# Kernel optimization log

Measured on AMD Instinct MI355X. Metric: run time of the kernel, lower is better.

## Reference

```python
import jax, jax.numpy as jnp
import numpy as np

L, D, OC, GROUPS, EPS = 256, 1280, 128, 8, 1e-5


def setup_inputs() -> dict:
    key = jax.random.key(0)
    k1, k2 = jax.random.split(key)
    feats = jax.random.normal(k1, (L, D), dtype=jnp.float32)
    # Conv2d(3d, out_ch, kernel_size=1) weight flattened to (out_ch, 3d)
    W = jax.random.normal(k2, (OC, 3 * D), dtype=jnp.float32) * (1.0 / np.sqrt(3 * D))
    b = jnp.zeros((OC,), dtype=jnp.float32)
    gamma = jnp.ones((OC,), dtype=jnp.float32)
    beta = jnp.zeros((OC,), dtype=jnp.float32)
    return {"feats": feats, "W": W, "b": b, "gamma": gamma, "beta": beta}


def reference(feats, W, b, gamma, beta):
    fi = feats[:, None, :]                     # (L, 1, d)
    fj = feats[None, :, :]                     # (1, L, d)
    add = fi + fj                              # (L, L, d)
    diff = jnp.abs(fi - fj)                    # (L, L, d)
    had = fi * fj                              # (L, L, d)
    pair = jnp.concatenate([add, diff, had], axis=-1)  # (L, L, 3d)
    # 1x1 conv == per-pixel linear: (L, L, 3d) x (out_ch, 3d)^T -> (L, L, out_ch)
    x = jnp.einsum('ijc,oc->ijo', pair, W) + b
    # GroupNorm(8, out_ch) on batch=1: normalize over (C/g, L, L) per group
    xg = jnp.transpose(x, (2, 0, 1)).reshape(GROUPS, OC // GROUPS, L, L)
    mean = jnp.mean(xg, axis=(1, 2, 3), keepdims=True)
    var = jnp.var(xg, axis=(1, 2, 3), keepdims=True)
    xn = ((xg - mean) * jax.lax.rsqrt(var + EPS)).reshape(OC, L, L)
    xn = xn * gamma[:, None, None] + beta[:, None, None]
    out = jax.nn.gelu(xn, approximate=False)   # torch nn.GELU default = exact erf
    return out[None]                           # (1, out_ch, L, L)
```

## Files before the change

### kernel.cpp

```cpp
#include <hip/hip_runtime.h>
#include <math.h>

typedef unsigned int uint;
typedef unsigned short ushort;

typedef __attribute__((ext_vector_type(8))) _Float16 f16x8;
typedef __attribute__((ext_vector_type(2))) _Float16 f16x2;
typedef __attribute__((ext_vector_type(16))) float floatx16;

#define NFEAT 327680
#define NWA   163840
#define NWP   327680

union U4H8 { uint4 u; f16x8 h; uint w[4]; };

__device__ inline ushort f2h(float f) {
  _Float16 h = (_Float16)f;
  union { _Float16 h; ushort s; } c; c.h = h; return c.s;
}
__device__ inline f16x2 asf16x2(uint u) {
  union { uint u; f16x2 h; } c; c.u = u; return c.h;
}
__device__ inline uint asuint(f16x2 h) {
  union { f16x2 h; uint u; } c; c.h = h; return c.u;
}

__global__ void prep_kernel(const float* __restrict__ feats,
                            const float* __restrict__ W,
                            ushort* __restrict__ fH,
                            ushort* __restrict__ wA,
                            ushort* __restrict__ wP,
                            float* __restrict__ stats,
                            float* __restrict__ Aoi) {
  int idx = blockIdx.x * 256 + threadIdx.x;
  if (blockIdx.x == 0 && threadIdx.x < 16) stats[threadIdx.x] = 0.0f;
  if (idx < 32768) Aoi[idx] = 0.0f;
  if (idx < NFEAT) {
    fH[idx] = f2h(feats[idx]);
  } else {
    const int e = idx - NFEAT;
    const int o = e / 3840;
    const int c = e - o * 3840;
    const ushort v = f2h(W[e]);
    if (c < 1280) {
      wA[o * 1280 + c] = v;
    } else {
      const int cp = c - 1280;
      const int t = cp / 1280;
      const int kk = cp - t * 1280;
      const int ks = kk >> 4;
      const int khalf = (kk >> 3) & 1;
      const int ko = kk & 7;
      const int lane = khalf * 32 + (o & 31);
      const int tile = (ks * 2 + t) * 4 + (o >> 5);
      wP[tile * 512 + lane * 8 + ko] = v;
    }
  }
}

__global__ __launch_bounds__(256, 2) void gemma_kernel(
    const ushort* __restrict__ fH, const ushort* __restrict__ wA,
    float* __restrict__ Aoi) {
  __shared__ float red[4][1024];
  const int tid = threadIdx.x, lane = tid & 63, w = tid >> 6;
  const int i0 = (blockIdx.x >> 4) << 5;
  const int kq = (blockIdx.x >> 2) & 3;
  const int ot = blockIdx.x & 3;
  const int rr = lane & 31, half = lane >> 5;
  floatx16 a4;
  #pragma unroll
  for (int r = 0; r < 16; ++r) a4[r] = 0.0f;
  const int kbase = kq * 320 + w * 80 + half * 8;
  #pragma unroll
  for (int ks = 0; ks < 5; ++ks) {
    const int k = kbase + ks * 16;
    U4H8 bf; bf.u = *(const uint4*)(fH + (i0 + rr) * 1280 + k);
    U4H8 af; af.u = *(const uint4*)(wA + (ot * 32 + rr) * 1280 + k);
    a4 = __builtin_amdgcn_mfma_f32_32x32x16_f16(af.h, bf.h, a4, 0, 0, 0);
  }
  #pragma unroll
  for (int r = 0; r < 16; ++r) {
    const int orow = (r & 3) + 8 * (r >> 2) + 4 * half;
    red[w][orow * 32 + rr] = a4[r];
  }
  __syncthreads();
  for (int e = tid; e < 1024; e += 256) {
    float s = red[0][e] + red[1][e] + red[2][e] + red[3][e];
    atomicAdd(&Aoi[(ot * 32 + (e >> 5)) * 256 + i0 + (e & 31)], s);
  }
}

__device__ inline void build_pair(const uint4 vj, const uint4 vi, U4H8& d, U4H8& h) {
  const uint ju[4] = {vj.x, vj.y, vj.z, vj.w};
  const uint iu[4] = {vi.x, vi.y, vi.z, vi.w};
  #pragma unroll
  for (int t = 0; t < 4; ++t) {
    f16x2 a = asf16x2(iu[t]);
    f16x2 b = asf16x2(ju[t]);
    f16x2 dd = a - b;
    f16x2 hh = a * b;
    d.w[t] = asuint(dd) & 0x7fff7fffu;
    h.w[t] = asuint(hh);
  }
}

__global__ __launch_bounds__(256, 2) void gemm_kernel(
    const ushort* __restrict__ fH, const ushort* __restrict__ wP,
    const float* __restrict__ bias, const float* __restrict__ Aoi,
    float* __restrict__ xout, float* __restrict__ stats) {
  __shared__ float sred[16];

  const int tid = threadIdx.x;
  const int blk = blockIdx.x;
  const int i0 = (blk >> 2) << 1;
  const int j0 = (blk & 3) << 6;
  const int lane = tid & 63;
  const int w = tid >> 6;
  const int wo = (w >> 1) << 6;
  const int wm = (w & 1) << 5;
  const int rr = lane & 31;
  const int half = lane >> 5;

  const ushort* wpl = wP + ((wo >> 5) << 9) + lane * 8;
  const ushort* fi0p = fH + i0 * 1280 + half * 8;
  const ushort* fi1p = fi0p + 1280;
  const ushort* fjp  = fH + (j0 + wm + rr) * 1280 + half * 8;

  floatx16 acc[2][2];
  #pragma unroll
  for (int a = 0; a < 2; ++a)
    #pragma unroll
    for (int ot = 0; ot < 2; ++ot)
      #pragma unroll
      for (int r = 0; r < 16; ++r) acc[a][ot][r] = 0.0f;

  U4H8 wfA[8], wfB[8];
  uint4 vjA[2], viA0[2], viA1[2], vjB[2], viB0[2], viB1[2];

#define CHUNK_LOAD(WF, VJ, VI0, VI1, CC) do {                                 \
    const int _b = (CC) * 16;                                                 \
    _Pragma("unroll")                                                         \
    for (int _q = 0; _q < 8; ++_q) {                                          \
      const int _st = _q >> 2, _t = (_q >> 1) & 1, _oi = _q & 1;              \
      (WF)[_q].u = *(const uint4*)(wpl + ((_b + _st * 8 + _t * 4 + _oi) << 9)); \
    }                                                                         \
    const int _cb = (CC) << 5;                                                \
    _Pragma("unroll")                                                         \
    for (int _s = 0; _s < 2; ++_s) {                                          \
      (VJ)[_s]  = *(const uint4*)(fjp  + _cb + _s * 16);                      \
      (VI0)[_s] = *(const uint4*)(fi0p + _cb + _s * 16);                      \
      (VI1)[_s] = *(const uint4*)(fi1p + _cb + _s * 16);                      \
    }                                                                         \
  } while (0)

#define CHUNK_COMPUTE(WF, VJ, VI0, VI1) do {                                  \
    _Pragma("unroll")                                                         \
    for (int _s = 0; _s < 2; ++_s) {                                          \
      U4H8 d0, h0, d1, h1;                                                    \
      build_pair((VJ)[_s], (VI0)[_s], d0, h0);                                \
      build_pair((VJ)[_s], (VI1)[_s], d1, h1);                                \
      acc[0][0] = __builtin_amdgcn_mfma_f32_32x32x16_f16((WF)[_s*4+0].h, d0.h, acc[0][0], 0, 0, 0); \
      acc[1][0] = __builtin_amdgcn_mfma_f32_32x32x16_f16((WF)[_s*4+0].h, d1.h, acc[1][0], 0, 0, 0); \
      acc[0][1] = __builtin_amdgcn_mfma_f32_32x32x16_f16((WF)[_s*4+1].h, d0.h, acc[0][1], 0, 0, 0); \
      acc[1][1] = __builtin_amdgcn_mfma_f32_32x32x16_f16((WF)[_s*4+1].h, d1.h, acc[1][1], 0, 0, 0); \
      acc[0][0] = __builtin_amdgcn_mfma_f32_32x32x16_f16((WF)[_s*4+2].h, h0.h, acc[0][0], 0, 0, 0); \
      acc[1][0] = __builtin_amdgcn_mfma_f32_32x32x16_f16((WF)[_s*4+2].h, h1.h, acc[1][0], 0, 0, 0); \
      acc[0][1] = __builtin_amdgcn_mfma_f32_32x32x16_f16((WF)[_s*4+3].h, h0.h, acc[0][1], 0, 0, 0); \
      acc[1][1] = __builtin_amdgcn_mfma_f32_32x32x16_f16((WF)[_s*4+3].h, h1.h, acc[1][1], 0, 0, 0); \
    }                                                                         \
  } while (0)

  CHUNK_LOAD(wfA, vjA, viA0, viA1, 0);
  #pragma unroll 1
  for (int cc = 0; cc < 40; cc += 2) {
    CHUNK_LOAD(wfB, vjB, viB0, viB1, cc + 1);
    CHUNK_COMPUTE(wfA, vjA, viA0, viA1);
    if (cc + 2 < 40)
      CHUNK_LOAD(wfA, vjA, viA0, viA1, cc + 2);
    CHUNK_COMPUTE(wfB, vjB, viB0, viB1);
  }
#undef CHUNK_LOAD
#undef CHUNK_COMPUTE

  float gs[2][2] = {{0.f, 0.f}, {0.f, 0.f}};
  float gq[2][2] = {{0.f, 0.f}, {0.f, 0.f}};
  const int jg = j0 + wm + rr;
  #pragma unroll
  for (int ii = 0; ii < 2; ++ii) {
    const int irow = i0 + ii;
    const int mglob = irow * 256 + jg;
    #pragma unroll
    for (int ot = 0; ot < 2; ++ot) {
      #pragma unroll
      for (int r = 0; r < 16; ++r) {
        const int orow = (r & 3) + 8 * (r >> 2) + 4 * half;
        const int o = wo + ot * 32 + orow;
        float x = acc[ii][ot][r] + Aoi[o * 256 + irow] + Aoi[o * 256 + jg] + bias[o];
        xout[o * 65536 + mglob] = x;
        gs[ot][r >> 3] += x;
        gq[ot][r >> 3] += x * x;
      }
    }
  }
  if (tid < 16) sred[tid] = 0.0f;
  __syncthreads();
  #pragma unroll
  for (int ot = 0; ot < 2; ++ot) {
    #pragma unroll
    for (int rg = 0; rg < 2; ++rg) {
      float s = gs[ot][rg], qv = gq[ot][rg];
      for (int off = 32; off > 0; off >>= 1) {
        s += __shfl_xor(s, off, 64);
        qv += __shfl_xor(qv, off, 64);
      }
      if (lane == 0) {
        const int g = (wo >> 4) + ot * 2 + rg;
        atomicAdd(&sred[g], s);
        atomicAdd(&sred[8 + g], qv);
      }
    }
  }
  __syncthreads();
  if (tid < 16) atomicAdd(&stats[tid], sred[tid]);
}

__global__ void norm_kernel(float* __restrict__ xout,
                            const float* __restrict__ stats,
                            const float* __restrict__ gamma,
                            const float* __restrict__ beta) {
  const int idx = blockIdx.x * 256 + threadIdx.x;
  const int e = idx << 2;
  const int o = e >> 16;
  const int g = o >> 4;
  const float invN = 1.0f / 1048576.0f;
  const float mean = stats[g] * invN;
  const float var = stats[8 + g] * invN - mean * mean;
  const float inv = rsqrtf(var + 1e-5f);
  const float ga = gamma[o], be = beta[o];
  float4 v = *(float4*)(xout + e);
  float* pv = &v.x;
  #pragma unroll
  for (int t = 0; t < 4; ++t) {
    float xn = (pv[t] - mean) * inv * ga + be;
    pv[t] = 0.5f * xn * (1.0f + erff(xn * 0.70710678118654752f));
  }
  *(float4*)(xout + e) = v;
}

extern "C" void kernel_launch(void* const* d_in, const int* in_sizes, int n_in,
                              void* d_out, int out_size, void* d_ws, size_t ws_size,
                              hipStream_t stream) {
  const float* feats = (const float*)d_in[0];
  const float* W     = (const float*)d_in[1];
  const float* bias  = (const float*)d_in[2];
  const float* gamma = (const float*)d_in[3];
  const float* beta  = (const float*)d_in[4];
  float* out = (float*)d_out;

  ushort* fH = (ushort*)d_ws;
  ushort* wA = fH + NFEAT;
  ushort* wP = wA + NWA;
  float* stats = (float*)(wP + NWP);
  float* Aoi = stats + 16;

  prep_kernel<<<3200, 256, 0, stream>>>(feats, W, fH, wA, wP, stats, Aoi);
  gemma_kernel<<<128, 256, 0, stream>>>(fH, wA, Aoi);
  gemm_kernel<<<512, 256, 0, stream>>>(fH, wP, bias, Aoi, out, stats);
  norm_kernel<<<8192, 256, 0, stream>>>(out, stats, gamma, beta);
}
```

Measured before the change: 144.4 us.

## Fuse GroupNorm+GELU into GEMM via cooperative grid sync, keeping tile in registers

Merges the normalization kernel into the GEMM kernel using a cooperative launch and grid-wide sync, so pre-norm values stay in accumulator registers instead of being written and reread from global memory. Blocks grow to 512 threads covering four i-rows each, halving the grid to 256 blocks so all can be co-resident. Saves a full-size output round trip and one launch, at the cost of a grid barrier, tighter launch bounds that may pressure registers, and live accumulators across the sync.

```diff
diff --git a/kernel.cpp b/kernel.cpp
--- a/kernel.cpp
+++ b/kernel.cpp
@@ -1,5 +1,8 @@
 #include <hip/hip_runtime.h>
+#include <hip/hip_cooperative_groups.h>
 #include <math.h>
+
+namespace cg = cooperative_groups;
 
 typedef unsigned int uint;
 typedef unsigned short ushort;
@@ -104,25 +107,29 @@
   }
 }
 
-__global__ __launch_bounds__(256, 2) void gemm_kernel(
+__global__ __launch_bounds__(512, 4) void gemm_kernel(
     const ushort* __restrict__ fH, const ushort* __restrict__ wP,
     const float* __restrict__ bias, const float* __restrict__ Aoi,
-    float* __restrict__ xout, float* __restrict__ stats) {
+    float* __restrict__ xout, float* __restrict__ stats,
+    const float* __restrict__ gamma, const float* __restrict__ beta) {
   __shared__ float sred[16];
 
   const int tid = threadIdx.x;
   const int blk = blockIdx.x;
-  const int i0 = (blk >> 2) << 1;
+  const int i0 = (blk >> 2) << 2;
   const int j0 = (blk & 3) << 6;
   const int lane = tid & 63;
   const int w = tid >> 6;
-  const int wo = (w >> 1) << 6;
-  const int wm = (w & 1) << 5;
+  const int p  = w >> 2;
+  const int ob = (w >> 1) & 1;
+  const int jb = w & 1;
+  const int wo = ob << 6;
+  const int wm = jb << 5;
   const int rr = lane & 31;
   const int half = lane >> 5;
 
   const ushort* wpl = wP + ((wo >> 5) << 9) + lane * 8;
-  const ushort* fi0p = fH + i0 * 1280 + half * 8;
+  const ushort* fi0p = fH + (i0 + p * 2) * 1280 + half * 8;
   const ushort* fi1p = fi0p + 1280;
   const ushort* fjp  = fH + (j0 + wm + rr) * 1280 + half * 8;
 
@@ -187,8 +194,7 @@
   const int jg = j0 + wm + rr;
   #pragma unroll
   for (int ii = 0; ii < 2; ++ii) {
-    const int irow = i0 + ii;
-    const int mglob = irow * 256 + jg;
+    const int irow = i0 + p * 2 + ii;
     #pragma unroll
     for (int ot = 0; ot < 2; ++ot) {
       #pragma unroll
@@ -196,7 +202,7 @@
         const int orow = (r & 3) + 8 * (r >> 2) + 4 * half;
         const int o = wo + ot * 32 + orow;
         float x = acc[ii][ot][r] + Aoi[o * 256 + irow] + Aoi[o * 256 + jg] + bias[o];
-        xout[o * 65536 + mglob] = x;
+        acc[ii][ot][r] = x;
         gs[ot][r >> 3] += x;
         gq[ot][r >> 3] += x * x;
       }
@@ -222,29 +228,37 @@
   }
   __syncthreads();
   if (tid < 16) atomicAdd(&stats[tid], sred[tid]);
-}
-
-__global__ void norm_kernel(float* __restrict__ xout,
-                            const float* __restrict__ stats,
-                            const float* __restrict__ gamma,
-                            const float* __restrict__ beta) {
-  const int idx = blockIdx.x * 256 + threadIdx.x;
-  const int e = idx << 2;
-  const int o = e >> 16;
-  const int g = o >> 4;
+
+  cg::this_grid().sync();
+
   const float invN = 1.0f / 1048576.0f;
-  const float mean = stats[g] * invN;
-  const float var = stats[8 + g] * invN - mean * mean;
-  const float inv = rsqrtf(var + 1e-5f);
-  const float ga = gamma[o], be = beta[o];
-  float4 v = *(float4*)(xout + e);
-  float* pv = &v.x;
-  #pragma unroll
-  for (int t = 0; t < 4; ++t) {
-    float xn = (pv[t] - mean) * inv * ga + be;
-    pv[t] = 0.5f * xn * (1.0f + erff(xn * 0.70710678118654752f));
-  }
-  *(float4*)(xout + e) = v;
+  float gmean[2][2], ginv[2][2];
+  #pragma unroll
+  for (int ot = 0; ot < 2; ++ot)
+    #pragma unroll
+    for (int rg = 0; rg < 2; ++rg) {
+      const int g = (wo >> 4) + ot * 2 + rg;
+      const float mean = stats[g] * invN;
+      const float var = stats[8 + g] * invN - mean * mean;
+      gmean[ot][rg] = mean;
+      ginv[ot][rg] = rsqrtf(var + 1e-5f);
+    }
+  #pragma unroll
+  for (int ii = 0; ii < 2; ++ii) {
+    const int irow = i0 + p * 2 + ii;
+    const int mglob = irow * 256 + jg;
+    #pragma unroll
+    for (int ot = 0; ot < 2; ++ot) {
+      #pragma unroll
+      for (int r = 0; r < 16; ++r) {
+        const int orow = (r & 3) + 8 * (r >> 2) + 4 * half;
+        const int o = wo + ot * 32 + orow;
+        float xn = (acc[ii][ot][r] - gmean[ot][r >> 3]) * ginv[ot][r >> 3] * gamma[o] + beta[o];
+        xout[o * 65536 + mglob] =
+            0.5f * xn * (1.0f + erff(xn * 0.70710678118654752f));
+      }
+    }
+  }
 }
 
 extern "C" void kernel_launch(void* const* d_in, const int* in_sizes, int n_in,
@@ -265,6 +279,8 @@
 
   prep_kernel<<<3200, 256, 0, stream>>>(feats, W, fH, wA, wP, stats, Aoi);
   gemma_kernel<<<128, 256, 0, stream>>>(fH, wA, Aoi);
-  gemm_kernel<<<512, 256, 0, stream>>>(fH, wP, bias, Aoi, out, stats);
-  norm_kernel<<<8192, 256, 0, stream>>>(out, stats, gamma, beta);
-}
+
+  void* args[] = {&fH, &wP, &bias, &Aoi, &out, &stats, &gamma, &beta};
+  hipLaunchCooperativeKernel((void*)gemm_kernel, dim3(256), dim3(512),
+                             args, 0, stream);
+}
```

Result: slower. 375.0 us (+159.7%).

## Enlarge per-wave GEMM tile to 2i x 64j x 64o for more register reuse

Applied to the files above, without the earlier changes.

Each wave now computes a 2x2 tile of i-rows by j-subblocks across two 32-output slices, doubling accumulators to 8 MFMA tiles. Each weight fragment and pair-feature build is reused across more MFMAs, cutting global weight/feature loads per FLOP. The block covers 4 i-rows, so the grid halves to 256 blocks, and launch bounds drop to 1 block/SM to allow more registers. The risk is lower occupancy and fewer blocks than CUs, which may hurt latency hiding and load balance.

```diff
diff --git a/kernel.cpp b/kernel.cpp
--- a/kernel.cpp
+++ b/kernel.cpp
@@ -104,7 +104,7 @@
   }
 }
 
-__global__ __launch_bounds__(256, 2) void gemm_kernel(
+__global__ __launch_bounds__(256, 1) void gemm_kernel(
     const ushort* __restrict__ fH, const ushort* __restrict__ wP,
     const float* __restrict__ bias, const float* __restrict__ Aoi,
     float* __restrict__ xout, float* __restrict__ stats) {
@@ -112,32 +112,37 @@
 
   const int tid = threadIdx.x;
   const int blk = blockIdx.x;
-  const int i0 = (blk >> 2) << 1;
-  const int j0 = (blk & 3) << 6;
   const int lane = tid & 63;
   const int w = tid >> 6;
-  const int wo = (w >> 1) << 6;
-  const int wm = (w & 1) << 5;
+  const int ip = w >> 1;
+  const int ot = w & 1;
+  const int i0 = (blk >> 2) * 4 + ip * 2;
+  const int j0 = (blk & 3) << 6;
+  const int wo = ot << 6;
   const int rr = lane & 31;
   const int half = lane >> 5;
 
   const ushort* wpl = wP + ((wo >> 5) << 9) + lane * 8;
   const ushort* fi0p = fH + i0 * 1280 + half * 8;
   const ushort* fi1p = fi0p + 1280;
-  const ushort* fjp  = fH + (j0 + wm + rr) * 1280 + half * 8;
-
-  floatx16 acc[2][2];
+  const ushort* fj0p = fH + (j0 + rr) * 1280 + half * 8;
+  const ushort* fj1p = fj0p + 32 * 1280;
+
+  floatx16 acc[2][2][2];
   #pragma unroll
   for (int a = 0; a < 2; ++a)
     #pragma unroll
-    for (int ot = 0; ot < 2; ++ot)
+    for (int b = 0; b < 2; ++b)
       #pragma unroll
-      for (int r = 0; r < 16; ++r) acc[a][ot][r] = 0.0f;
+      for (int c = 0; c < 2; ++c)
+        #pragma unroll
+        for (int r = 0; r < 16; ++r) acc[a][b][c][r] = 0.0f;
 
   U4H8 wfA[8], wfB[8];
-  uint4 vjA[2], viA0[2], viA1[2], vjB[2], viB0[2], viB1[2];
-
-#define CHUNK_LOAD(WF, VJ, VI0, VI1, CC) do {                                 \
+  uint4 vj0A[2], vj1A[2], vi0A[2], vi1A[2];
+  uint4 vj0B[2], vj1B[2], vi0B[2], vi1B[2];
+
+#define CHUNK_LOAD(WF, VJ0, VJ1, VI0, VI1, CC) do {                           \
     const int _b = (CC) * 16;                                                 \
     _Pragma("unroll")                                                         \
     for (int _q = 0; _q < 8; ++_q) {                                          \
@@ -147,74 +152,85 @@
     const int _cb = (CC) << 5;                                                \
     _Pragma("unroll")                                                         \
     for (int _s = 0; _s < 2; ++_s) {                                          \
-      (VJ)[_s]  = *(const uint4*)(fjp  + _cb + _s * 16);                      \
+      (VJ0)[_s] = *(const uint4*)(fj0p + _cb + _s * 16);                      \
+      (VJ1)[_s] = *(const uint4*)(fj1p + _cb + _s * 16);                      \
       (VI0)[_s] = *(const uint4*)(fi0p + _cb + _s * 16);                      \
       (VI1)[_s] = *(const uint4*)(fi1p + _cb + _s * 16);                      \
     }                                                                         \
   } while (0)
 
-#define CHUNK_COMPUTE(WF, VJ, VI0, VI1) do {                                  \
+#define CHUNK_COMPUTE(WF, VJ0, VJ1, VI0, VI1) do {                            \
     _Pragma("unroll")                                                         \
     for (int _s = 0; _s < 2; ++_s) {                                          \
-      U4H8 d0, h0, d1, h1;                                                    \
-      build_pair((VJ)[_s], (VI0)[_s], d0, h0);                                \
-      build_pair((VJ)[_s], (VI1)[_s], d1, h1);                                \
-      acc[0][0] = __builtin_amdgcn_mfma_f32_32x32x16_f16((WF)[_s*4+0].h, d0.h, acc[0][0], 0, 0, 0); \
-      acc[1][0] = __builtin_amdgcn_mfma_f32_32x32x16_f16((WF)[_s*4+0].h, d1.h, acc[1][0], 0, 0, 0); \
-      acc[0][1] = __builtin_amdgcn_mfma_f32_32x32x16_f16((WF)[_s*4+1].h, d0.h, acc[0][1], 0, 0, 0); \
-      acc[1][1] = __builtin_amdgcn_mfma_f32_32x32x16_f16((WF)[_s*4+1].h, d1.h, acc[1][1], 0, 0, 0); \
-      acc[0][0] = __builtin_amdgcn_mfma_f32_32x32x16_f16((WF)[_s*4+2].h, h0.h, acc[0][0], 0, 0, 0); \
-      acc[1][0] = __builtin_amdgcn_mfma_f32_32x32x16_f16((WF)[_s*4+2].h, h1.h, acc[1][0], 0, 0, 0); \
-      acc[0][1] = __builtin_amdgcn_mfma_f32_32x32x16_f16((WF)[_s*4+3].h, h0.h, acc[0][1], 0, 0, 0); \
-      acc[1][1] = __builtin_amdgcn_mfma_f32_32x32x16_f16((WF)[_s*4+3].h, h1.h, acc[1][1], 0, 0, 0); \
+      U4H8 d00, h00, d01, h01, d10, h10, d11, h11;                            \
+      build_pair((VJ0)[_s], (VI0)[_s], d00, h00);                             \
+      build_pair((VJ0)[_s], (VI1)[_s], d01, h01);                             \
+      build_pair((VJ1)[_s], (VI0)[_s], d10, h10);                             \
+      build_pair((VJ1)[_s], (VI1)[_s], d11, h11);                             \
+      _Pragma("unroll")                                                       \
+      for (int _oi = 0; _oi < 2; ++_oi) {                                     \
+        const f16x8 wd = (WF)[_s * 4 + _oi].h;                                \
+        const f16x8 wh = (WF)[_s * 4 + 2 + _oi].h;                            \
+        acc[0][0][_oi] = __builtin_amdgcn_mfma_f32_32x32x16_f16(wd, d00.h, acc[0][0][_oi], 0, 0, 0); \
+        acc[1][0][_oi] = __builtin_amdgcn_mfma_f32_32x32x16_f16(wd, d01.h, acc[1][0][_oi], 0, 0, 0); \
+        acc[0][1][_oi] = __builtin_amdgcn_mfma_f32_32x32x16_f16(wd, d10.h, acc[0][1][_oi], 0, 0, 0); \
+        acc[1][1][_oi] = __builtin_amdgcn_mfma_f32_32x32x16_f16(wd, d11.h, acc[1][1][_oi], 0, 0, 0); \
+        acc[0][0][_oi] = __builtin_amdgcn_mfma_f32_32x32x16_f16(wh, h00.h, acc[0][0][_oi], 0, 0, 0); \
+        acc[1][0][_oi] = __builtin_amdgcn_mfma_f32_32x32x16_f16(wh, h01.h, acc[1][0][_oi], 0, 0, 0); \
+        acc[0][1][_oi] = __builtin_amdgcn_mfma_f32_32x32x16_f16(wh, h10.h, acc[0][1][_oi], 0, 0, 0); \
+        acc[1][1][_oi] = __builtin_amdgcn_mfma_f32_32x32x16_f16(wh, h11.h, acc[1][1][_oi], 0, 0, 0); \
+      }                                                                       \
     }                                                                         \
   } while (0)
 
-  CHUNK_LOAD(wfA, vjA, viA0, viA1, 0);
+  CHUNK_LOAD(wfA, vj0A, vj1A, vi0A, vi1A, 0);
   #pragma unroll 1
   for (int cc = 0; cc < 40; cc += 2) {
-    CHUNK_LOAD(wfB, vjB, viB0, viB1, cc + 1);
-    CHUNK_COMPUTE(wfA, vjA, viA0, viA1);
+    CHUNK_LOAD(wfB, vj0B, vj1B, vi0B, vi1B, cc + 1);
+    CHUNK_COMPUTE(wfA, vj0A, vj1A, vi0A, vi1A);
     if (cc + 2 < 40)
-      CHUNK_LOAD(wfA, vjA, viA0, viA1, cc + 2);
-    CHUNK_COMPUTE(wfB, vjB, viB0, viB1);
+      CHUNK_LOAD(wfA, vj0A, vj1A, vi0A, vi1A, cc + 2);
+    CHUNK_COMPUTE(wfB, vj0B, vj1B, vi0B, vi1B);
   }
 #undef CHUNK_LOAD
 #undef CHUNK_COMPUTE
 
   float gs[2][2] = {{0.f, 0.f}, {0.f, 0.f}};
   float gq[2][2] = {{0.f, 0.f}, {0.f, 0.f}};
-  const int jg = j0 + wm + rr;
   #pragma unroll
   for (int ii = 0; ii < 2; ++ii) {
     const int irow = i0 + ii;
-    const int mglob = irow * 256 + jg;
     #pragma unroll
-    for (int ot = 0; ot < 2; ++ot) {
+    for (int js = 0; js < 2; ++js) {
+      const int jg = j0 + js * 32 + rr;
+      const int mglob = irow * 256 + jg;
       #pragma unroll
-      for (int r = 0; r < 16; ++r) {
-        const int orow = (r & 3) + 8 * (r >> 2) + 4 * half;
-        const int o = wo + ot * 32 + orow;
-        float x = acc[ii][ot][r] + Aoi[o * 256 + irow] + Aoi[o * 256 + jg] + bias[o];
-        xout[o * 65536 + mglob] = x;
-        gs[ot][r >> 3] += x;
-        gq[ot][r >> 3] += x * x;
+      for (int oi = 0; oi < 2; ++oi) {
+        #pragma unroll
+        for (int r = 0; r < 16; ++r) {
+          const int orow = (r & 3) + 8 * (r >> 2) + 4 * half;
+          const int o = wo + oi * 32 + orow;
+          float x = acc[ii][js][oi][r] + Aoi[o * 256 + irow] + Aoi[o * 256 + jg] + bias[o];
+          xout[o * 65536 + mglob] = x;
+          gs[oi][r >> 3] += x;
+          gq[oi][r >> 3] += x * x;
+        }
       }
     }
   }
   if (tid < 16) sred[tid] = 0.0f;
   __syncthreads();
   #pragma unroll
-  for (int ot = 0; ot < 2; ++ot) {
+  for (int oi = 0; oi < 2; ++oi) {
     #pragma unroll
     for (int rg = 0; rg < 2; ++rg) {
-      float s = gs[ot][rg], qv = gq[ot][rg];
+      float s = gs[oi][rg], qv = gq[oi][rg];
       for (int off = 32; off > 0; off >>= 1) {
         s += __shfl_xor(s, off, 64);
         qv += __shfl_xor(qv, off, 64);
       }
       if (lane == 0) {
-        const int g = (wo >> 4) + ot * 2 + rg;
+        const int g = (wo >> 4) + oi * 2 + rg;
         atomicAdd(&sred[g], s);
         atomicAdd(&sred[8 + g], qv);
       }
@@ -265,6 +281,6 @@
 
   prep_kernel<<<3200, 256, 0, stream>>>(feats, W, fH, wA, wP, stats, Aoi);
   gemma_kernel<<<128, 256, 0, stream>>>(fH, wA, Aoi);
-  gemm_kernel<<<512, 256, 0, stream>>>(fH, wP, bias, Aoi, out, stats);
+  gemm_kernel<<<256, 256, 0, stream>>>(fH, wP, bias, Aoi, out, stats);
   norm_kernel<<<8192, 256, 0, stream>>>(out, stats, gamma, beta);
 }
```

After: 146.6 us. About the same (+1.6%).
